# Kernel optimization log

Measured on AMD Instinct MI355X. Metric: run time of the kernel, lower is better.

The kernel has to match this reference:

```python
import jax, jax.numpy as jnp
import numpy as np

B, H, S, D = 4, 16, 2048, 128

def setup_inputs() -> dict:
    key = jax.random.key(0)
    kq, kk, kv = jax.random.split(key, 3)
    query = jax.random.normal(kq, (B, H, S, D), dtype=jnp.float32)
    k = jax.random.normal(kk, (B, H, S, D), dtype=jnp.float32)
    v = jax.random.normal(kv, (B, H, S, D), dtype=jnp.float32)
    # causal mask: True = masked (not attended), broadcastable to (B,H,S,S)
    mask = jnp.triu(jnp.ones((S, S), dtype=bool), k=1)[None, None, :, :]
    return {"query": query, "key": k, "value": v, "mask": mask}

def reference(query, key, value, mask):
    d_k = query.shape[-1]
    scale = 1.0 / np.sqrt(d_k).astype(np.float32)
    # scores: (B,H,Sq,Sk)
    scores = jnp.einsum('bhqd,bhkd->bhqk', query, key) * scale
    scores = jnp.where(mask, -jnp.inf, scores)
    attention_weights = jax.nn.softmax(scores, axis=-1)
    output = jnp.einsum('bhqk,bhkd->bhqd', attention_weights, value)
    return output, attention_weights
```

## Files before the change

kernel.cpp:

```cpp
#include <hip/hip_runtime.h>
#include <hip/hip_bf16.h>

#define B_ 4
#define H_ 16
#define S_ 2048
#define D_ 128

typedef unsigned short u16;
typedef unsigned int u32;

typedef __attribute__((ext_vector_type(8))) short bf16x8;
typedef __attribute__((ext_vector_type(4))) float f32x4;
typedef __attribute__((ext_vector_type(4))) unsigned short u16x4;

__device__ __forceinline__ float bf2f(u16 x) {
    return __uint_as_float(((u32)x) << 16);
}

__device__ __forceinline__ u16 f2bf(float f) {
    u32 u = __float_as_uint(f);
    u32 lsb = (u >> 16) & 1u;
    u += 0x7fffu + lsb;
    return (u16)(u >> 16);
}

__global__ void detect_dtype_kernel(const u32* __restrict__ q, int* __restrict__ flag) {
    __shared__ int cnt;
    if (threadIdx.x == 0) cnt = 0;
    __syncthreads();
    int c = 0;
    for (int i = threadIdx.x; i < 4096; i += 256) {
        float lo = bf2f((u16)(q[i] & 0xffffu));
        if (!(fabsf(lo) <= 64.0f)) c++;
    }
    atomicAdd(&cnt, c);
    __syncthreads();
    if (threadIdx.x == 0) *flag = (cnt > 256) ? 1 : 0;
}

__global__ __launch_bounds__(256) void attn_bf16_kernel(
    const u16* __restrict__ Q, const u16* __restrict__ K, const u16* __restrict__ V,
    u16* __restrict__ Out, u16* __restrict__ W, const int* __restrict__ flag)
{
    if (*flag != 0) return;

    __shared__ float qs[D_];
    __shared__ float sc[S_];
    __shared__ float red[8];
    __shared__ float ot[512];

    const int tid = threadIdx.x;
    for (int idx = blockIdx.x; idx < B_ * H_ * S_; idx += (int)gridDim.x) {
        const int q   = idx & (S_ - 1);
        const int bh  = idx >> 11;
        const size_t rowQ = (size_t)idx * D_;
        const u16* Kb = K + (size_t)bh * S_ * D_;
        const u16* Vb = V + (size_t)bh * S_ * D_;
        const int nk = q + 1;
        const float scale = 0.08838834764831845f;

        if (tid < D_) qs[tid] = bf2f(Q[rowQ + tid]) * scale;
        __syncthreads();

        float lmax = -1e30f;
        for (int k = tid; k < nk; k += 256) {
            const uint4* K4 = reinterpret_cast<const uint4*>(Kb + (size_t)k * D_);
            float acc = 0.f;
            #pragma unroll
            for (int c = 0; c < D_ / 8; ++c) {
                uint4 u = K4[c];
                const int d = c * 8;
                acc += qs[d + 0] * bf2f((u16)(u.x & 0xffffu));
                acc += qs[d + 1] * bf2f((u16)(u.x >> 16));
                acc += qs[d + 2] * bf2f((u16)(u.y & 0xffffu));
                acc += qs[d + 3] * bf2f((u16)(u.y >> 16));
                acc += qs[d + 4] * bf2f((u16)(u.z & 0xffffu));
                acc += qs[d + 5] * bf2f((u16)(u.z >> 16));
                acc += qs[d + 6] * bf2f((u16)(u.w & 0xffffu));
                acc += qs[d + 7] * bf2f((u16)(u.w >> 16));
            }
            sc[k] = acc;
            lmax = fmaxf(lmax, acc);
        }

        #pragma unroll
        for (int off = 32; off > 0; off >>= 1)
            lmax = fmaxf(lmax, __shfl_down(lmax, off, 64));
        if ((tid & 63) == 0) red[tid >> 6] = lmax;
        __syncthreads();
        const float mx = fmaxf(fmaxf(red[0], red[1]), fmaxf(red[2], red[3]));

        float lsum = 0.f;
        for (int k = tid; k < nk; k += 256) {
            float e = __expf(sc[k] - mx);
            sc[k] = e;
            lsum += e;
        }
        #pragma unroll
        for (int off = 32; off > 0; off >>= 1)
            lsum += __shfl_down(lsum, off, 64);
        if ((tid & 63) == 0) red[4 + (tid >> 6)] = lsum;
        __syncthreads();
        const float rsum = 1.0f / (red[4] + red[5] + red[6] + red[7]);

        u32* Wrow2 = reinterpret_cast<u32*>(W + (size_t)idx * S_);
        for (int k2 = tid; k2 < S_ / 2; k2 += 256) {
            const int k0 = 2 * k2, k1 = 2 * k2 + 1;
            float w0 = (k0 < nk) ? sc[k0] * rsum : 0.f;
            float w1 = (k1 < nk) ? sc[k1] * rsum : 0.f;
            if (k0 < nk) sc[k0] = w0;
            if (k1 < nk) sc[k1] = w1;
            Wrow2[k2] = (u32)f2bf(w0) | ((u32)f2bf(w1) << 16);
        }
        __syncthreads();

        const int d2   = tid & 63;
        const int part = tid >> 6;
        const u32* V2 = reinterpret_cast<const u32*>(Vb);
        float a0 = 0.f, a1 = 0.f;
        for (int k = part; k < nk; k += 4) {
            const u32 u = V2[(size_t)k * (D_ / 2) + d2];
            const float w = sc[k];
            a0 += w * bf2f((u16)(u & 0xffffu));
            a1 += w * bf2f((u16)(u >> 16));
        }
        ot[part * D_ + 2 * d2]     = a0;
        ot[part * D_ + 2 * d2 + 1] = a1;
        __syncthreads();

        if (tid < D_) {
            const float o = ot[tid] + ot[D_ + tid] + ot[2 * D_ + tid] + ot[3 * D_ + tid];
            Out[rowQ + tid] = f2bf(o);
        }
        __syncthreads();
    }
}

__global__ __launch_bounds__(256) void split_qk_kernel(
    const float* __restrict__ Q, const float* __restrict__ K,
    u16* __restrict__ Qh, u16* __restrict__ Ql,
    u16* __restrict__ Kh, u16* __restrict__ Kl,
    const int* __restrict__ flag)
{
    if (*flag != 1) return;
    const float scale = 0.08838834764831845f;
    const int N4 = (B_ * H_ * S_ * D_) / 4;
    const float4* Q4 = reinterpret_cast<const float4*>(Q);
    const float4* K4 = reinterpret_cast<const float4*>(K);
    for (int g = blockIdx.x * 256 + threadIdx.x; g < N4; g += 2048 * 256) {
        {
            float4 v = Q4[g];
            float s0 = v.x * scale, s1 = v.y * scale, s2 = v.z * scale, s3 = v.w * scale;
            u16 h0 = f2bf(s0), h1 = f2bf(s1), h2 = f2bf(s2), h3 = f2bf(s3);
            u16x4 hv = {h0, h1, h2, h3};
            u16x4 lv = {f2bf(s0 - bf2f(h0)), f2bf(s1 - bf2f(h1)),
                        f2bf(s2 - bf2f(h2)), f2bf(s3 - bf2f(h3))};
            *reinterpret_cast<u16x4*>(&Qh[(size_t)4 * g]) = hv;
            *reinterpret_cast<u16x4*>(&Ql[(size_t)4 * g]) = lv;
        }
        {
            float4 v = K4[g];
            u16 h0 = f2bf(v.x), h1 = f2bf(v.y), h2 = f2bf(v.z), h3 = f2bf(v.w);
            u16x4 hv = {h0, h1, h2, h3};
            u16x4 lv = {f2bf(v.x - bf2f(h0)), f2bf(v.y - bf2f(h1)),
                        f2bf(v.z - bf2f(h2)), f2bf(v.w - bf2f(h3))};
            *reinterpret_cast<u16x4*>(&Kh[(size_t)4 * g]) = hv;
            *reinterpret_cast<u16x4*>(&Kl[(size_t)4 * g]) = lv;
        }
    }
}

__global__ __launch_bounds__(256) void transpose_v_kernel(
    const float* __restrict__ V, u16* __restrict__ VT, const int* __restrict__ flag)
{
    if (*flag != 1) return;
    __shared__ float ts[64 * 130];
    const int tid = threadIdx.x;
    const int bh = blockIdx.x >> 5;
    const int kt = blockIdx.x & 31;
    const int k0 = kt * 64;
    const float4* V4 = reinterpret_cast<const float4*>(V + ((size_t)bh * S_ + k0) * D_);
    #pragma unroll
    for (int it = 0; it < 8; ++it) {
        int g = tid + 256 * it;
        int r = g >> 5, c4 = g & 31;
        float4 v = V4[g];
        ts[r * 130 + 4 * c4 + 0] = v.x;
        ts[r * 130 + 4 * c4 + 1] = v.y;
        ts[r * 130 + 4 * c4 + 2] = v.z;
        ts[r * 130 + 4 * c4 + 3] = v.w;
    }
    __syncthreads();
    const int d = tid >> 1, kh2 = tid & 1;
    u16* dst = VT + (size_t)bh * (D_ * S_) + (size_t)d * S_ + k0 + 32 * kh2;
    #pragma unroll
    for (int jj = 0; jj < 4; ++jj) {
        bf16x8 o;
        #pragma unroll
        for (int j = 0; j < 8; ++j) {
            int k = 32 * kh2 + 8 * jj + j;
            o[j] = (short)f2bf(ts[k * 130 + d]);
        }
        *reinterpret_cast<bf16x8*>(&dst[8 * jj]) = o;
    }
}

__global__ __launch_bounds__(256, 3) void attn_mfma_kernel(
    const u16* __restrict__ Qh, const u16* __restrict__ Ql,
    const u16* __restrict__ Kh, const u16* __restrict__ Kl,
    const u16* __restrict__ VT,
    float* __restrict__ Out, float* __restrict__ W, const int* __restrict__ flag)
{
    if (*flag != 1) return;

    __shared__ __align__(16) short qh_s[32 * 128];
    __shared__ __align__(16) short ql_s[32 * 128];
    __shared__ __align__(16) short kh_s[32 * 128];
    __shared__ __align__(16) short kl_s[32 * 128];
    __shared__ __align__(16) short vt_s[128 * 32];
    __shared__ __align__(16) float e_s[32 * 36];
    __shared__ float red2[2][32];
    __shared__ float rinv_s[32];

    const int tid = threadIdx.x;
    const int w   = tid >> 6;
    const int l   = tid & 63;
    const int l15 = l & 15;
    const int l4  = l >> 4;
    const int fq  = w >> 1;
    const int fk  = w & 1;

    const int bidx = blockIdx.x;
    const int bh   = bidx >> 6;
    const int qt   = 63 - (bidx & 63);
    const int q0   = qt << 5;
    const int nkt  = qt + 1;

    const u16* QhB = Qh + ((size_t)bh * S_ + q0) * D_;
    const u16* QlB = Ql + ((size_t)bh * S_ + q0) * D_;
    const u16* KhB = Kh + (size_t)bh * S_ * D_;
    const u16* KlB = Kl + (size_t)bh * S_ * D_;
    const u16* VTB = VT + (size_t)bh * (size_t)D_ * S_;
    float* Ob = Out + ((size_t)bh * S_ + q0) * D_;
    float* Wb = W + ((size_t)bh * S_ + q0) * (size_t)S_;

    #pragma unroll
    for (int it = 0; it < 2; ++it) {
        int g = tid + 256 * it;
        int r = g >> 4, ch = g & 15;
        bf16x8 a = *reinterpret_cast<const bf16x8*>(&QhB[(size_t)r * D_ + 8 * ch]);
        bf16x8 b = *reinterpret_cast<const bf16x8*>(&QlB[(size_t)r * D_ + 8 * ch]);
        int li = r * 128 + ((8 * ch) ^ ((r & 7) << 3));
        *reinterpret_cast<bf16x8*>(&qh_s[li]) = a;
        *reinterpret_cast<bf16x8*>(&ql_s[li]) = b;
    }

    const int qrow = 16 * fq + l15;
    const int qx   = (qrow & 7) << 3;
    const int krow = 16 * fk + l15;
    const int kx   = (krow & 7) << 3;
    const int col0 = 8 * l4;

    f32x4 oacc[4];
    #pragma unroll
    for (int nb = 0; nb < 4; ++nb) { oacc[nb] = {0.f, 0.f, 0.f, 0.f}; }
    float rs[4] = {0.f, 0.f, 0.f, 0.f};

    for (int kt2 = 0; kt2 < nkt; ++kt2) {
        const int k0 = kt2 << 5;
        #pragma unroll
        for (int it = 0; it < 2; ++it) {
            int g = tid + 256 * it;
            int r = g >> 4, ch = g & 15;
            bf16x8 a = *reinterpret_cast<const bf16x8*>(&KhB[(size_t)(k0 + r) * D_ + 8 * ch]);
            bf16x8 b = *reinterpret_cast<const bf16x8*>(&KlB[(size_t)(k0 + r) * D_ + 8 * ch]);
            int d = g >> 2, c2 = g & 3;
            bf16x8 c = *reinterpret_cast<const bf16x8*>(&VTB[(size_t)d * S_ + k0 + 8 * c2]);
            int li = r * 128 + ((8 * ch) ^ ((r & 7) << 3));
            *reinterpret_cast<bf16x8*>(&kh_s[li]) = a;
            *reinterpret_cast<bf16x8*>(&kl_s[li]) = b;
            *reinterpret_cast<bf16x8*>(&vt_s[d * 32 + 8 * (c2 ^ (d & 3))]) = c;
        }
        __syncthreads();

        f32x4 acc = {0.f, 0.f, 0.f, 0.f};
        #pragma unroll
        for (int ks = 0; ks < 4; ++ks) {
            int ca = 32 * ks + col0;
            bf16x8 aH = *reinterpret_cast<const bf16x8*>(&qh_s[qrow * 128 + (ca ^ qx)]);
            bf16x8 aL = *reinterpret_cast<const bf16x8*>(&ql_s[qrow * 128 + (ca ^ qx)]);
            bf16x8 bH = *reinterpret_cast<const bf16x8*>(&kh_s[krow * 128 + (ca ^ kx)]);
            bf16x8 bL = *reinterpret_cast<const bf16x8*>(&kl_s[krow * 128 + (ca ^ kx)]);
            acc = __builtin_amdgcn_mfma_f32_16x16x32_bf16(aH, bH, acc, 0, 0, 0);
            acc = __builtin_amdgcn_mfma_f32_16x16x32_bf16(aH, bL, acc, 0, 0, 0);
            acc = __builtin_amdgcn_mfma_f32_16x16x32_bf16(aL, bH, acc, 0, 0, 0);
        }

        #pragma unroll
        for (int i = 0; i < 4; ++i) {
            int row = 16 * fq + 4 * l4 + i;
            int col = 16 * fk + l15;
            float e = 0.f;
            if (k0 + col <= q0 + row) e = __expf(acc[i]);
            rs[i] += e;
            e_s[row * 36 + col] = e;
        }
        __syncthreads();

        bf16x8 aP;
        {
            const float* pr = &e_s[(16 * fq + l15) * 36 + col0];
            float4 p0 = *reinterpret_cast<const float4*>(pr);
            float4 p1 = *reinterpret_cast<const float4*>(pr + 4);
            aP[0] = (short)f2bf(p0.x); aP[1] = (short)f2bf(p0.y);
            aP[2] = (short)f2bf(p0.z); aP[3] = (short)f2bf(p0.w);
            aP[4] = (short)f2bf(p1.x); aP[5] = (short)f2bf(p1.y);
            aP[6] = (short)f2bf(p1.z); aP[7] = (short)f2bf(p1.w);
        }
        #pragma unroll
        for (int nb = 0; nb < 4; ++nb) {
            int dcol = 64 * fk + 16 * nb + l15;
            bf16x8 bV = *reinterpret_cast<const bf16x8*>(&vt_s[dcol * 32 + 8 * (l4 ^ (dcol & 3))]);
            oacc[nb] = __builtin_amdgcn_mfma_f32_16x16x32_bf16(aP, bV, oacc[nb], 0, 0, 0);
        }
        __syncthreads();
    }

    #pragma unroll
    for (int i = 0; i < 4; ++i) {
        float v = rs[i];
        v += __shfl_xor(v, 1, 64);
        v += __shfl_xor(v, 2, 64);
        v += __shfl_xor(v, 4, 64);
        v += __shfl_xor(v, 8, 64);
        if (l15 == 0) red2[fk][16 * fq + 4 * l4 + i] = v;
    }
    __syncthreads();
    if (tid < 32) rinv_s[tid] = 1.0f / (red2[0][tid] + red2[1][tid]);
    __syncthreads();

    #pragma unroll
    for (int nb = 0; nb < 4; ++nb) {
        #pragma unroll
        for (int i = 0; i < 4; ++i) {
            int row = 16 * fq + 4 * l4 + i;
            int col = 64 * fk + 16 * nb + l15;
            Ob[(size_t)row * D_ + col] = oacc[nb][i] * rinv_s[row];
        }
    }

    for (int kt2 = 0; kt2 < nkt; ++kt2) {
        const int k0 = kt2 << 5;
        #pragma unroll
        for (int it = 0; it < 2; ++it) {
            int g = tid + 256 * it;
            int r = g >> 4, ch = g & 15;
            bf16x8 a = *reinterpret_cast<const bf16x8*>(&KhB[(size_t)(k0 + r) * D_ + 8 * ch]);
            bf16x8 b = *reinterpret_cast<const bf16x8*>(&KlB[(size_t)(k0 + r) * D_ + 8 * ch]);
            int li = r * 128 + ((8 * ch) ^ ((r & 7) << 3));
            *reinterpret_cast<bf16x8*>(&kh_s[li]) = a;
            *reinterpret_cast<bf16x8*>(&kl_s[li]) = b;
        }
        __syncthreads();

        f32x4 acc = {0.f, 0.f, 0.f, 0.f};
        #pragma unroll
        for (int ks = 0; ks < 4; ++ks) {
            int ca = 32 * ks + col0;
            bf16x8 aH = *reinterpret_cast<const bf16x8*>(&qh_s[qrow * 128 + (ca ^ qx)]);
            bf16x8 aL = *reinterpret_cast<const bf16x8*>(&ql_s[qrow * 128 + (ca ^ qx)]);
            bf16x8 bH = *reinterpret_cast<const bf16x8*>(&kh_s[krow * 128 + (ca ^ kx)]);
            bf16x8 bL = *reinterpret_cast<const bf16x8*>(&kl_s[krow * 128 + (ca ^ kx)]);
            acc = __builtin_amdgcn_mfma_f32_16x16x32_bf16(aH, bH, acc, 0, 0, 0);
            acc = __builtin_amdgcn_mfma_f32_16x16x32_bf16(aH, bL, acc, 0, 0, 0);
            acc = __builtin_amdgcn_mfma_f32_16x16x32_bf16(aL, bH, acc, 0, 0, 0);
        }

        #pragma unroll
        for (int i = 0; i < 4; ++i) {
            int row = 16 * fq + 4 * l4 + i;
            int col = 16 * fk + l15;
            float e = 0.f;
            if (k0 + col <= q0 + row) e = __expf(acc[i]) * rinv_s[row];
            e_s[row * 36 + col] = e;
        }
        __syncthreads();

        {
            int row = tid >> 3, c4 = tid & 7;
            f32x4 wv = *reinterpret_cast<const f32x4*>(&e_s[row * 36 + 4 * c4]);
            __builtin_nontemporal_store(wv,
                reinterpret_cast<f32x4*>(Wb + (size_t)row * S_ + k0 + 4 * c4));
        }
        __syncthreads();
    }

    const int kend = nkt << 5;
    const f32x4 z4 = {0.f, 0.f, 0.f, 0.f};
    for (int g = tid; g < 32 * (S_ / 4); g += 256) {
        int row = g >> 9, c4g = g & 511;
        if ((c4g << 2) >= kend)
            __builtin_nontemporal_store(z4,
                reinterpret_cast<f32x4*>(Wb + (size_t)row * S_ + 4 * c4g));
    }
}

#define BQ 32
#define BK 64
#define LSTR 33
#define ESTR 68

__device__ __forceinline__ void dot4(float& a, const float4& x, const float4& y) {
    a = fmaf(x.x, y.x, a); a = fmaf(x.y, y.y, a);
    a = fmaf(x.z, y.z, a); a = fmaf(x.w, y.w, a);
}
__device__ __forceinline__ void fma4(float4& a, float s, const float4& b) {
    a.x = fmaf(s, b.x, a.x); a.y = fmaf(s, b.y, a.y);
    a.z = fmaf(s, b.z, a.z); a.w = fmaf(s, b.w, a.w);
}

__global__ __launch_bounds__(256) void attn_f32_tiled(
    const float* __restrict__ Q, const float* __restrict__ K, const float* __restrict__ V,
    float* __restrict__ Out, float* __restrict__ W, const int* __restrict__ flag)
{
    if (*flag != 1) return;

    __shared__ float4 qs4[BQ * LSTR];
    __shared__ float4 kv4[BK * LSTR];
    __shared__ __align__(16) float e_s[BQ * ESTR];
    __shared__ float rsum_s[BQ];
    __shared__ float rinv_s[BQ];

    const int tid  = threadIdx.x;
    const int bidx = blockIdx.x;
    const int bh   = bidx >> 6;
    const int qt   = 63 - (bidx & 63);
    const int q0   = qt << 5;
    const int nkt  = ((q0 + BQ - 1) >> 6) + 1;
    const float scale = 0.08838834764831845f;

    const float* Kb = K + (size_t)bh * (S_ * D_);
    const float* Vb = V + (size_t)bh * (S_ * D_);
    const float* Qb = Q + ((size_t)bh * S_ + q0) * D_;
    float* Ob = Out + ((size_t)bh * S_ + q0) * D_;
    float* Wb = W + ((size_t)bh * S_ + q0) * (size_t)S_;

    const int rgq = tid >> 4;
    const int cgq = tid & 15;
    const int rg = tid >> 4;
    const int cg = tid & 15;

    {
        const float4* Qg = reinterpret_cast<const float4*>(Qb);
        #pragma unroll
        for (int t = 0; t < 4; ++t) {
            const int g = tid + 256 * t;
            qs4[(g >> 5) * LSTR + (g & 31)] = Qg[g];
        }
        const float4* Kg = reinterpret_cast<const float4*>(Kb);
        #pragma unroll
        for (int t = 0; t < 8; ++t) {
            const int g = tid + 256 * t;
            kv4[(g >> 5) * LSTR + (g & 31)] = Kg[g];
        }
    }
    __syncthreads();

    float4 o4[2][2] = {};
    float rsf[2] = {0.f, 0.f};

    for (int kt = 0; kt < nkt; ++kt) {
        const int k0 = kt << 6;
        const bool more = (kt + 1 < nkt);

        float4 vreg[8];
        {
            const float4* Vg = reinterpret_cast<const float4*>(Vb) + (size_t)k0 * 32;
            #pragma unroll
            for (int t = 0; t < 8; ++t) vreg[t] = Vg[tid + 256 * t];
        }

        float acc[2][4] = {};
        {
            const int qb0 = (rgq * 2 + 0) * LSTR;
            const int qb1 = (rgq * 2 + 1) * LSTR;
            const int kb0 = (cgq +  0) * LSTR;
            const int kb1 = (cgq + 16) * LSTR;
            const int kb2 = (cgq + 32) * LSTR;
            const int kb3 = (cgq + 48) * LSTR;
            #pragma unroll 4
            for (int d4 = 0; d4 < 32; ++d4) {
                const float4 qv0 = qs4[qb0 + d4];
                const float4 qv1 = qs4[qb1 + d4];
                const float4 kv0 = kv4[kb0 + d4];
                const float4 kv1 = kv4[kb1 + d4];
                const float4 kv2 = kv4[kb2 + d4];
                const float4 kv3 = kv4[kb3 + d4];
                dot4(acc[0][0], qv0, kv0); dot4(acc[0][1], qv0, kv1);
                dot4(acc[0][2], qv0, kv2); dot4(acc[0][3], qv0, kv3);
                dot4(acc[1][0], qv1, kv0); dot4(acc[1][1], qv1, kv1);
                dot4(acc[1][2], qv1, kv2); dot4(acc[1][3], qv1, kv3);
            }
        }

        #pragma unroll
        for (int i = 0; i < 2; ++i) {
            const int r  = rgq * 2 + i;
            const int qg = q0 + r;
            float* Wrow = Wb + (size_t)r * S_ + k0;
            #pragma unroll
            for (int j = 0; j < 4; ++j) {
                const int kc = cgq + 16 * j;
                const float e = (k0 + kc <= qg) ? __expf(acc[i][j] * scale) : 0.0f;
                rsf[i] += e;
                e_s[r * ESTR + kc] = e;
                Wrow[kc] = e;
            }
        }
        __syncthreads();

        #pragma unroll
        for (int t = 0; t < 8; ++t) {
            const int g = tid + 256 * t;
            kv4[(g >> 5) * LSTR + (g & 31)] = vreg[t];
        }
        float4 kreg[8];
        if (more) {
            const float4* Kg = reinterpret_cast<const float4*>(Kb) + (size_t)(k0 + BK) * 32;
            #pragma unroll
            for (int t = 0; t < 8; ++t) kreg[t] = Kg[tid + 256 * t];
        }
        __syncthreads();

        {
            const int eb0 = (rg * 2 + 0) * ESTR;
            const int eb1 = (rg * 2 + 1) * ESTR;
            #pragma unroll 2
            for (int kk = 0; kk < BK; kk += 4) {
                const float4 e0 = *reinterpret_cast<const float4*>(&e_s[eb0 + kk]);
                const float4 e1 = *reinterpret_cast<const float4*>(&e_s[eb1 + kk]);
                const float ea[4] = {e0.x, e0.y, e0.z, e0.w};
                const float eb[4] = {e1.x, e1.y, e1.z, e1.w};
                #pragma unroll
                for (int t = 0; t < 4; ++t) {
                    const float4 v0 = kv4[(kk + t) * LSTR + cg];
                    const float4 v1 = kv4[(kk + t) * LSTR + 16 + cg];
                    fma4(o4[0][0], ea[t], v0);
                    fma4(o4[0][1], ea[t], v1);
                    fma4(o4[1][0], eb[t], v0);
                    fma4(o4[1][1], eb[t], v1);
                }
            }
        }

        if (more) {
            __syncthreads();
            #pragma unroll
            for (int t = 0; t < 8; ++t) {
                const int g = tid + 256 * t;
                kv4[(g >> 5) * LSTR + (g & 31)] = kreg[t];
            }
            __syncthreads();
        }
    }

    #pragma unroll
    for (int i = 0; i < 2; ++i) {
        float v = rsf[i];
        v += __shfl_xor(v, 8, 64);
        v += __shfl_xor(v, 4, 64);
        v += __shfl_xor(v, 2, 64);
        v += __shfl_xor(v, 1, 64);
        if (cgq == 0) rsum_s[rgq * 2 + i] = v;
    }
    __syncthreads();
    if (tid < BQ) rinv_s[tid] = 1.0f / rsum_s[tid];
    __syncthreads();

    #pragma unroll
    for (int i = 0; i < 2; ++i) {
        const int r = rg * 2 + i;
        const float inv = rinv_s[r];
        float4 a = o4[i][0];
        a.x *= inv; a.y *= inv; a.z *= inv; a.w *= inv;
        float4 b = o4[i][1];
        b.x *= inv; b.y *= inv; b.z *= inv; b.w *= inv;
        float4* Orow = reinterpret_cast<float4*>(Ob + (size_t)r * D_);
        Orow[cg]      = a;
        Orow[16 + cg] = b;
    }

    {
        const int kend = nkt << 6;
        float4* W4 = reinterpret_cast<float4*>(Wb);
        for (int g = tid; g < BQ * (S_ / 4); g += 256) {
            const int row = g >> 9;
            const int c4  = g & 511;
            const size_t off = (size_t)row * (S_ / 4) + c4;
            if ((c4 << 2) < kend) {
                float4 wv = W4[off];
                const float inv = rinv_s[row];
                wv.x *= inv; wv.y *= inv; wv.z *= inv; wv.w *= inv;
                W4[off] = wv;
            } else {
                W4[off] = make_float4(0.f, 0.f, 0.f, 0.f);
            }
        }
    }
}

extern "C" void kernel_launch(void* const* d_in, const int* in_sizes, int n_in,
                              void* d_out, int out_size, void* d_ws, size_t ws_size,
                              hipStream_t stream) {
    int* flag = (int*)d_ws;

    detect_dtype_kernel<<<dim3(1), dim3(256), 0, stream>>>((const u32*)d_in[0], flag);

    {
        const u16* Q = (const u16*)d_in[0];
        const u16* K = (const u16*)d_in[1];
        const u16* V = (const u16*)d_in[2];
        u16* Out = (u16*)d_out;
        u16* Wp  = Out + (size_t)B_ * H_ * S_ * D_;
        attn_bf16_kernel<<<dim3(2048), dim3(256), 0, stream>>>(Q, K, V, Out, Wp, flag);
    }

    const size_t PLSZ = (size_t)B_ * H_ * S_ * D_;
    const size_t NEED = 256 + 5 * PLSZ * sizeof(u16);
    float* OutF = (float*)d_out;
    float* WF   = OutF + PLSZ;

    if (ws_size >= NEED) {
        u16* base = (u16*)((char*)d_ws + 256);
        u16* Qh = base;
        u16* Ql = Qh + PLSZ;
        u16* Kh = Ql + PLSZ;
        u16* Kl = Kh + PLSZ;
        u16* VTp = Kl + PLSZ;
        split_qk_kernel<<<dim3(2048), dim3(256), 0, stream>>>(
            (const float*)d_in[0], (const float*)d_in[1], Qh, Ql, Kh, Kl, flag);
        transpose_v_kernel<<<dim3(2048), dim3(256), 0, stream>>>(
            (const float*)d_in[2], VTp, flag);
        attn_mfma_kernel<<<dim3(B_ * H_ * (S_ / 32)), dim3(256), 0, stream>>>(
            Qh, Ql, Kh, Kl, VTp, OutF, WF, flag);
    } else {
        attn_f32_tiled<<<dim3(B_ * H_ * (S_ / 32)), dim3(256), 0, stream>>>(
            (const float*)d_in[0], (const float*)d_in[1], (const float*)d_in[2],
            OutF, WF, flag);
    }
}
```

Measured before the change: 1.937 ms.

## Write unnormalized weights in one pass, then rescale in place; 64-wide K tiles with register prefetch

The second QK^T recompute pass is replaced: the first pass stores the unnormalized exponentials to W directly, and a final sweep reads W back, scales each row by its inverse sum and zero-fills the masked tail. The key tile grows from 32 to 64 columns, and the next K/V tile is prefetched into registers during compute. This removes half of the QK MFMA work and the second K stream, at the cost of a read-modify-write of W through global memory. Occupancy drops from 3 to 2 blocks per CU because of the larger shared buffers.

Result: no change. 1.918 ms (-1.0%).

```diff
diff --git a/kernel.cpp b/kernel.cpp
--- a/kernel.cpp
+++ b/kernel.cpp
@@ -205,7 +205,9 @@
     }
 }
 
-__global__ __launch_bounds__(256, 3) void attn_mfma_kernel(
+#define ESTR 68
+
+__global__ __launch_bounds__(256, 2) void attn_mfma_kernel(
     const u16* __restrict__ Qh, const u16* __restrict__ Ql,
     const u16* __restrict__ Kh, const u16* __restrict__ Kl,
     const u16* __restrict__ VT,
@@ -215,10 +217,10 @@
 
     __shared__ __align__(16) short qh_s[32 * 128];
     __shared__ __align__(16) short ql_s[32 * 128];
-    __shared__ __align__(16) short kh_s[32 * 128];
-    __shared__ __align__(16) short kl_s[32 * 128];
-    __shared__ __align__(16) short vt_s[128 * 32];
-    __shared__ __align__(16) float e_s[32 * 36];
+    __shared__ __align__(16) short kh_s[64 * 128];
+    __shared__ __align__(16) short kl_s[64 * 128];
+    __shared__ __align__(16) short vt_s[128 * 64];
+    __shared__ __align__(16) float e_s[32 * ESTR];
     __shared__ float red2[2][32];
     __shared__ float rinv_s[32];
 
@@ -234,7 +236,7 @@
     const int bh   = bidx >> 6;
     const int qt   = 63 - (bidx & 63);
     const int q0   = qt << 5;
-    const int nkt  = qt + 1;
+    const int nkt  = (q0 + 95) >> 6;
 
     const u16* QhB = Qh + ((size_t)bh * S_ + q0) * D_;
     const u16* QlB = Ql + ((size_t)bh * S_ + q0) * D_;
@@ -257,8 +259,6 @@
 
     const int qrow = 16 * fq + l15;
     const int qx   = (qrow & 7) << 3;
-    const int krow = 16 * fk + l15;
-    const int kx   = (krow & 7) << 3;
     const int col0 = 8 * l4;
 
     f32x4 oacc[4];
@@ -266,62 +266,104 @@
     for (int nb = 0; nb < 4; ++nb) { oacc[nb] = {0.f, 0.f, 0.f, 0.f}; }
     float rs[4] = {0.f, 0.f, 0.f, 0.f};
 
-    for (int kt2 = 0; kt2 < nkt; ++kt2) {
-        const int k0 = kt2 << 5;
-        #pragma unroll
-        for (int it = 0; it < 2; ++it) {
+    bf16x8 rkh[4], rkl[4], rvt[4];
+    {
+        #pragma unroll
+        for (int it = 0; it < 4; ++it) {
+            int g = tid + 256 * it;
+            rkh[it] = *reinterpret_cast<const bf16x8*>(&KhB[(size_t)(g >> 4) * D_ + 8 * (g & 15)]);
+            rkl[it] = *reinterpret_cast<const bf16x8*>(&KlB[(size_t)(g >> 4) * D_ + 8 * (g & 15)]);
+            rvt[it] = *reinterpret_cast<const bf16x8*>(&VTB[(size_t)(g >> 3) * S_ + 8 * (g & 7)]);
+        }
+    }
+
+    for (int kt = 0; kt < nkt; ++kt) {
+        const int k0 = kt << 6;
+
+        #pragma unroll
+        for (int it = 0; it < 4; ++it) {
             int g = tid + 256 * it;
             int r = g >> 4, ch = g & 15;
-            bf16x8 a = *reinterpret_cast<const bf16x8*>(&KhB[(size_t)(k0 + r) * D_ + 8 * ch]);
-            bf16x8 b = *reinterpret_cast<const bf16x8*>(&KlB[(size_t)(k0 + r) * D_ + 8 * ch]);
-            int d = g >> 2, c2 = g & 3;
-            bf16x8 c = *reinterpret_cast<const bf16x8*>(&VTB[(size_t)d * S_ + k0 + 8 * c2]);
             int li = r * 128 + ((8 * ch) ^ ((r & 7) << 3));
-            *reinterpret_cast<bf16x8*>(&kh_s[li]) = a;
-            *reinterpret_cast<bf16x8*>(&kl_s[li]) = b;
-            *reinterpret_cast<bf16x8*>(&vt_s[d * 32 + 8 * (c2 ^ (d & 3))]) = c;
-        }
-        __syncthreads();
-
-        f32x4 acc = {0.f, 0.f, 0.f, 0.f};
-        #pragma unroll
-        for (int ks = 0; ks < 4; ++ks) {
-            int ca = 32 * ks + col0;
-            bf16x8 aH = *reinterpret_cast<const bf16x8*>(&qh_s[qrow * 128 + (ca ^ qx)]);
-            bf16x8 aL = *reinterpret_cast<const bf16x8*>(&ql_s[qrow * 128 + (ca ^ qx)]);
-            bf16x8 bH = *reinterpret_cast<const bf16x8*>(&kh_s[krow * 128 + (ca ^ kx)]);
-            bf16x8 bL = *reinterpret_cast<const bf16x8*>(&kl_s[krow * 128 + (ca ^ kx)]);
-            acc = __builtin_amdgcn_mfma_f32_16x16x32_bf16(aH, bH, acc, 0, 0, 0);
-            acc = __builtin_amdgcn_mfma_f32_16x16x32_bf16(aH, bL, acc, 0, 0, 0);
-            acc = __builtin_amdgcn_mfma_f32_16x16x32_bf16(aL, bH, acc, 0, 0, 0);
-        }
-
-        #pragma unroll
-        for (int i = 0; i < 4; ++i) {
-            int row = 16 * fq + 4 * l4 + i;
-            int col = 16 * fk + l15;
-            float e = 0.f;
-            if (k0 + col <= q0 + row) e = __expf(acc[i]);
-            rs[i] += e;
-            e_s[row * 36 + col] = e;
-        }
-        __syncthreads();
-
-        bf16x8 aP;
-        {
-            const float* pr = &e_s[(16 * fq + l15) * 36 + col0];
-            float4 p0 = *reinterpret_cast<const float4*>(pr);
-            float4 p1 = *reinterpret_cast<const float4*>(pr + 4);
-            aP[0] = (short)f2bf(p0.x); aP[1] = (short)f2bf(p0.y);
-            aP[2] = (short)f2bf(p0.z); aP[3] = (short)f2bf(p0.w);
-            aP[4] = (short)f2bf(p1.x); aP[5] = (short)f2bf(p1.y);
-            aP[6] = (short)f2bf(p1.z); aP[7] = (short)f2bf(p1.w);
-        }
-        #pragma unroll
-        for (int nb = 0; nb < 4; ++nb) {
-            int dcol = 64 * fk + 16 * nb + l15;
-            bf16x8 bV = *reinterpret_cast<const bf16x8*>(&vt_s[dcol * 32 + 8 * (l4 ^ (dcol & 3))]);
-            oacc[nb] = __builtin_amdgcn_mfma_f32_16x16x32_bf16(aP, bV, oacc[nb], 0, 0, 0);
+            *reinterpret_cast<bf16x8*>(&kh_s[li]) = rkh[it];
+            *reinterpret_cast<bf16x8*>(&kl_s[li]) = rkl[it];
+            int d = g >> 3, c8 = g & 7;
+            *reinterpret_cast<bf16x8*>(&vt_s[d * 64 + 8 * (c8 ^ (d & 7))]) = rvt[it];
+        }
+        __syncthreads();
+
+        if (kt + 1 < nkt) {
+            const int kn = k0 + 64;
+            #pragma unroll
+            for (int it = 0; it < 4; ++it) {
+                int g = tid + 256 * it;
+                rkh[it] = *reinterpret_cast<const bf16x8*>(&KhB[(size_t)(kn + (g >> 4)) * D_ + 8 * (g & 15)]);
+                rkl[it] = *reinterpret_cast<const bf16x8*>(&KlB[(size_t)(kn + (g >> 4)) * D_ + 8 * (g & 15)]);
+                rvt[it] = *reinterpret_cast<const bf16x8*>(&VTB[(size_t)(g >> 3) * S_ + kn + 8 * (g & 7)]);
+            }
+        }
+
+        f32x4 acc2[2];
+        acc2[0] = {0.f, 0.f, 0.f, 0.f};
+        acc2[1] = {0.f, 0.f, 0.f, 0.f};
+        #pragma unroll
+        for (int nb = 0; nb < 2; ++nb) {
+            const int krow = 32 * fk + 16 * nb + l15;
+            const int kx   = (krow & 7) << 3;
+            #pragma unroll
+            for (int ks = 0; ks < 4; ++ks) {
+                int ca = 32 * ks + col0;
+                bf16x8 aH = *reinterpret_cast<const bf16x8*>(&qh_s[qrow * 128 + (ca ^ qx)]);
+                bf16x8 aL = *reinterpret_cast<const bf16x8*>(&ql_s[qrow * 128 + (ca ^ qx)]);
+                bf16x8 bH = *reinterpret_cast<const bf16x8*>(&kh_s[krow * 128 + (ca ^ kx)]);
+                bf16x8 bL = *reinterpret_cast<const bf16x8*>(&kl_s[krow * 128 + (ca ^ kx)]);
+                acc2[nb] = __builtin_amdgcn_mfma_f32_16x16x32_bf16(aH, bH, acc2[nb], 0, 0, 0);
+                acc2[nb] = __builtin_amdgcn_mfma_f32_16x16x32_bf16(aH, bL, acc2[nb], 0, 0, 0);
+                acc2[nb] = __builtin_amdgcn_mfma_f32_16x16x32_bf16(aL, bH, acc2[nb], 0, 0, 0);
+            }
+        }
+
+        #pragma unroll
+        for (int nb = 0; nb < 2; ++nb) {
+            #pragma unroll
+            for (int i = 0; i < 4; ++i) {
+                int row = 16 * fq + 4 * l4 + i;
+                int col = 32 * fk + 16 * nb + l15;
+                float e = 0.f;
+                if (k0 + col <= q0 + row) e = __expf(acc2[nb][i]);
+                rs[i] += e;
+                e_s[row * ESTR + col] = e;
+            }
+        }
+        __syncthreads();
+
+        #pragma unroll
+        for (int t = 0; t < 2; ++t) {
+            int idx = tid + 256 * t;
+            int row = idx >> 4, c4 = idx & 15;
+            f32x4 wv = *reinterpret_cast<const f32x4*>(&e_s[row * ESTR + 4 * c4]);
+            *reinterpret_cast<f32x4*>(Wb + (size_t)row * S_ + k0 + 4 * c4) = wv;
+        }
+
+        #pragma unroll
+        for (int ks2 = 0; ks2 < 2; ++ks2) {
+            bf16x8 aP;
+            {
+                const float* pr = &e_s[(16 * fq + l15) * ESTR + 32 * ks2 + col0];
+                float4 p0 = *reinterpret_cast<const float4*>(pr);
+                float4 p1 = *reinterpret_cast<const float4*>(pr + 4);
+                aP[0] = (short)f2bf(p0.x); aP[1] = (short)f2bf(p0.y);
+                aP[2] = (short)f2bf(p0.z); aP[3] = (short)f2bf(p0.w);
+                aP[4] = (short)f2bf(p1.x); aP[5] = (short)f2bf(p1.y);
+                aP[6] = (short)f2bf(p1.z); aP[7] = (short)f2bf(p1.w);
+            }
+            #pragma unroll
+            for (int nb = 0; nb < 4; ++nb) {
+                int dcol = 64 * fk + 16 * nb + l15;
+                bf16x8 bV = *reinterpret_cast<const bf16x8*>(
+                    &vt_s[dcol * 64 + 8 * ((4 * ks2 + l4) ^ (dcol & 7))]);
+                oacc[nb] = __builtin_amdgcn_mfma_f32_16x16x32_bf16(aP, bV, oacc[nb], 0, 0, 0);
+            }
         }
         __syncthreads();
     }
@@ -349,66 +391,30 @@
         }
     }
 
-    for (int kt2 = 0; kt2 < nkt; ++kt2) {
-        const int k0 = kt2 << 5;
-        #pragma unroll
-        for (int it = 0; it < 2; ++it) {
-            int g = tid + 256 * it;
-            int r = g >> 4, ch = g & 15;
-            bf16x8 a = *reinterpret_cast<const bf16x8*>(&KhB[(size_t)(k0 + r) * D_ + 8 * ch]);
-            bf16x8 b = *reinterpret_cast<const bf16x8*>(&KlB[(size_t)(k0 + r) * D_ + 8 * ch]);
-            int li = r * 128 + ((8 * ch) ^ ((r & 7) << 3));
-            *reinterpret_cast<bf16x8*>(&kh_s[li]) = a;
-            *reinterpret_cast<bf16x8*>(&kl_s[li]) = b;
-        }
-        __syncthreads();
-
-        f32x4 acc = {0.f, 0.f, 0.f, 0.f};
-        #pragma unroll
-        for (int ks = 0; ks < 4; ++ks) {
-            int ca = 32 * ks + col0;
-            bf16x8 aH = *reinterpret_cast<const bf16x8*>(&qh_s[qrow * 128 + (ca ^ qx)]);
-            bf16x8 aL = *reinterpret_cast<const bf16x8*>(&ql_s[qrow * 128 + (ca ^ qx)]);
-            bf16x8 bH = *reinterpret_cast<const bf16x8*>(&kh_s[krow * 128 + (ca ^ kx)]);
-            bf16x8 bL = *reinterpret_cast<const bf16x8*>(&kl_s[krow * 128 + (ca ^ kx)]);
-            acc = __builtin_amdgcn_mfma_f32_16x16x32_bf16(aH, bH, acc, 0, 0, 0);
-            acc = __builtin_amdgcn_mfma_f32_16x16x32_bf16(aH, bL, acc, 0, 0, 0);
-            acc = __builtin_amdgcn_mfma_f32_16x16x32_bf16(aL, bH, acc, 0, 0, 0);
-        }
-
-        #pragma unroll
-        for (int i = 0; i < 4; ++i) {
-            int row = 16 * fq + 4 * l4 + i;
-            int col = 16 * fk + l15;
-            float e = 0.f;
-            if (k0 + col <= q0 + row) e = __expf(acc[i]) * rinv_s[row];
-            e_s[row * 36 + col] = e;
-        }
-        __syncthreads();
-
-        {
-            int row = tid >> 3, c4 = tid & 7;
-            f32x4 wv = *reinterpret_cast<const f32x4*>(&e_s[row * 36 + 4 * c4]);
-            __builtin_nontemporal_store(wv,
-                reinterpret_cast<f32x4*>(Wb + (size_t)row * S_ + k0 + 4 * c4));
-        }
-        __syncthreads();
-    }
-
-    const int kend = nkt << 5;
-    const f32x4 z4 = {0.f, 0.f, 0.f, 0.f};
-    for (int g = tid; g < 32 * (S_ / 4); g += 256) {
-        int row = g >> 9, c4g = g & 511;
-        if ((c4g << 2) >= kend)
-            __builtin_nontemporal_store(z4,
-                reinterpret_cast<f32x4*>(Wb + (size_t)row * S_ + 4 * c4g));
+    {
+        const int kend = nkt << 6;
+        f32x4* W4 = reinterpret_cast<f32x4*>(Wb);
+        const f32x4 z4 = {0.f, 0.f, 0.f, 0.f};
+        for (int g = tid; g < 32 * (S_ / 4); g += 256) {
+            const int row = g >> 9;
+            const int c4  = g & 511;
+            const size_t off = (size_t)row * (S_ / 4) + c4;
+            if ((c4 << 2) < kend) {
+                f32x4 wv = W4[off];
+                const float inv = rinv_s[row];
+                wv.x *= inv; wv.y *= inv; wv.z *= inv; wv.w *= inv;
+                W4[off] = wv;
+            } else {
+                __builtin_nontemporal_store(z4, &W4[off]);
+            }
+        }
     }
 }
 
 #define BQ 32
 #define BK 64
 #define LSTR 33
-#define ESTR 68
+#define FESTR 68
 
 __device__ __forceinline__ void dot4(float& a, const float4& x, const float4& y) {
     a = fmaf(x.x, y.x, a); a = fmaf(x.y, y.y, a);
@@ -427,7 +433,7 @@
 
     __shared__ float4 qs4[BQ * LSTR];
     __shared__ float4 kv4[BK * LSTR];
-    __shared__ __align__(16) float e_s[BQ * ESTR];
+    __shared__ __align__(16) float e_s[BQ * FESTR];
     __shared__ float rsum_s[BQ];
     __shared__ float rinv_s[BQ];
 
@@ -513,7 +519,7 @@
                 const int kc = cgq + 16 * j;
                 const float e = (k0 + kc <= qg) ? __expf(acc[i][j] * scale) : 0.0f;
                 rsf[i] += e;
-                e_s[r * ESTR + kc] = e;
+                e_s[r * FESTR + kc] = e;
                 Wrow[kc] = e;
             }
         }
@@ -533,8 +539,8 @@
         __syncthreads();
 
         {
-            const int eb0 = (rg * 2 + 0) * ESTR;
-            const int eb1 = (rg * 2 + 1) * ESTR;
+            const int eb0 = (rg * 2 + 0) * FESTR;
+            const int eb1 = (rg * 2 + 1) * FESTR;
             #pragma unroll 2
             for (int kk = 0; kk < BK; kk += 4) {
                 const float4 e0 = *reinterpret_cast<const float4*>(&e_s[eb0 + kk]);
```
